# Optimization experiments

Hardware: AMD Instinct MI355X
Metric: run time of the kernel (lower is better)

Reference implementation:

```python
import jax, jax.numpy as jnp
import numpy as np

T, B, D, H = 1024, 256, 64, 128  # seq_len, batch, x_dim, dim_RNN (= dense dims)


def _linear_params(key, fan_in, fan_out):
    # torch nn.Linear/nn.RNN default init: U(-1/sqrt(fan_in), 1/sqrt(fan_in))
    s = 1.0 / np.sqrt(fan_in)
    kw, kb = jax.random.split(key)
    W = jax.random.uniform(kw, (fan_out, fan_in), minval=-s, maxval=s, dtype=jnp.float32)
    b = jax.random.uniform(kb, (fan_out,), minval=-s, maxval=s, dtype=jnp.float32)
    return W, b


def setup_inputs() -> dict:
    key = jax.random.key(0)
    kx, k1, k2, k3, k4, k5 = jax.random.split(key, 6)
    x = jax.random.normal(kx, (T, B, D), dtype=jnp.float32)
    W_x, b_x = _linear_params(k1, D, H)      # feature_extractor_x: Linear(D->H)
    W_ih, b_ih = _linear_params(k2, H, H)    # RNN input-hidden
    W_hh, b_hh = _linear_params(k3, H, H)    # RNN hidden-hidden
    W_h, b_h = _linear_params(k4, H, H)      # mlp_h_x: Linear(H->H)
    W_g, b_g = _linear_params(k5, H, D)      # gen_out: Linear(H->D)
    return {"x": x, "W_x": W_x, "b_x": b_x, "W_ih": W_ih, "b_ih": b_ih,
            "W_hh": W_hh, "b_hh": b_hh, "W_h": W_h, "b_h": b_h,
            "W_g": W_g, "b_g": b_g}


def reference(x, W_x, b_x, W_ih, b_ih, W_hh, b_hh, W_h, b_h, W_g, b_g):
    # feature extractor applied to all timesteps at once (as in the original)
    feat = jnp.tanh(x @ W_x.T + b_x)                       # [T, B, H]
    batch = x.shape[1]
    h0 = jnp.zeros((batch, W_hh.shape[0]), dtype=x.dtype)  # [B, H]

    def step(h, f_t):
        # y_t is produced from h BEFORE the recurrence update (y[0] uses h=0)
        y_t = jnp.tanh(h @ W_h.T + b_h) @ W_g.T + b_g      # [B, D]
        h_next = jnp.tanh(f_t @ W_ih.T + b_ih + h @ W_hh.T + b_hh)
        return h_next, y_t

    _, y = jax.lax.scan(step, h0, feat)                    # y: [T, B, D]
    return y
```

## Files before the change

### kernel.cpp

```cpp
#include <hip/hip_runtime.h>


#define T_SEQ 1024
#define B_SZ  256
#define D_IN  64
#define H_DIM 128

typedef __attribute__((ext_vector_type(8))) _Float16 half8;
typedef __attribute__((ext_vector_type(4))) _Float16 half4;
typedef __attribute__((ext_vector_type(4))) float f32x4;

__device__ __forceinline__ float fast_tanh(float x) {
  float ax = __builtin_fabsf(x);
  float e  = __builtin_amdgcn_exp2f(ax * -2.8853900817779268f);
  float r  = (1.0f - e) * __builtin_amdgcn_rcpf(1.0f + e);
  return __builtin_copysignf(r, x);
}

__device__ __forceinline__ void barrier_lds_only() {
  __asm__ __volatile__("" ::: "memory");
  __builtin_amdgcn_s_waitcnt(0xC07F);
  __builtin_amdgcn_s_barrier();
  __asm__ __volatile__("" ::: "memory");
}

__device__ __forceinline__ half8 pack_h8(float4 a, float4 b) {
  half8 s = { (_Float16)a.x, (_Float16)a.y, (_Float16)a.z, (_Float16)a.w,
              (_Float16)b.x, (_Float16)b.y, (_Float16)b.z, (_Float16)b.w };
  return s;
}

__device__ __forceinline__ float add_xor1(float x) {
  int v = __builtin_amdgcn_mov_dpp(__float_as_int(x), 0xB1, 0xF, 0xF, true);
  return x + __int_as_float(v);
}
__device__ __forceinline__ float add_xor2(float x) {
  int v = __builtin_amdgcn_mov_dpp(__float_as_int(x), 0x4E, 0xF, 0xF, true);
  return x + __int_as_float(v);
}
__device__ __forceinline__ float add_mirror8(float x) {
  int v = __builtin_amdgcn_mov_dpp(__float_as_int(x), 0x141, 0xF, 0xF, true);
  return x + __int_as_float(v);
}
__device__ __forceinline__ float dot4(float4 w, float4 h) {
  return fmaf(w.x, h.x, fmaf(w.y, h.y, fmaf(w.z, h.z, w.w * h.w)));
}

#define WI_S 136
#define XT_S 72
#define FM_S 136

__global__ __launch_bounds__(256) void k_feat_mfma(
    const float* __restrict__ x,  const float* __restrict__ Wx,
    const float* __restrict__ bx, const float* __restrict__ Wih,
    const float* __restrict__ bih,const float* __restrict__ bhh,
    float* __restrict__ Z)
{
  __shared__ __align__(16) _Float16 wi_l[128 * WI_S];
  __shared__ __align__(16) _Float16 xt_l[64 * XT_S];
  __shared__ __align__(16) _Float16 fm_l[64 * FM_S];

  const int tid = threadIdx.x;
  const int l   = tid & 63;
  const int wv  = tid >> 6;
  const int ln  = l & 15;
  const int kg  = l >> 4;

  {
    const float4* w4 = (const float4*)Wih;
#pragma unroll
    for (int p = 0; p < 16; ++p) {
      int f = tid + p * 256;
      int row = f >> 5, kc = (f & 31) * 4;
      float4 v = w4[f];
      half4 s = { (_Float16)v.x, (_Float16)v.y, (_Float16)v.z, (_Float16)v.w };
      *(half4*)&wi_l[row * WI_S + kc] = s;
    }
  }
  half8 wxr[8][2];
#pragma unroll
  for (int nt = 0; nt < 8; ++nt)
#pragma unroll
    for (int kf = 0; kf < 2; ++kf) {
      const float* wp = Wx + (nt*16 + ln) * D_IN + kf*32 + kg*8;
      wxr[nt][kf] = pack_h8(*(const float4*)wp, *(const float4*)(wp + 4));
    }

  float bx_r[8], b2_r[8];
#pragma unroll
  for (int nt = 0; nt < 8; ++nt) {
    bx_r[nt] = bx[nt*16 + ln];
    b2_r[nt] = bih[nt*16 + ln] + bhh[nt*16 + ln];
  }

  for (int it = 0; it < 8; ++it) {
    const long tile = blockIdx.x * 8 + it;
    const long r0   = tile * 64;

    {
      const float4* x4 = (const float4*)x;
#pragma unroll
      for (int p = 0; p < 4; ++p) {
        int f = tid + p * 256;
        int row = f >> 4, kc = (f & 15) * 4;
        float4 v = x4[r0 * 16 + f];
        half4 s = { (_Float16)v.x, (_Float16)v.y, (_Float16)v.z, (_Float16)v.w };
        *(half4*)&xt_l[row * XT_S + kc] = s;
      }
    }
    barrier_lds_only();

    half8 a1[2];
#pragma unroll
    for (int kf = 0; kf < 2; ++kf)
      a1[kf] = *(const half8*)&xt_l[(wv*16 + ln) * XT_S + kf*32 + kg*8];

#pragma unroll
    for (int nt = 0; nt < 8; ++nt) {
      f32x4 acc = {0.f, 0.f, 0.f, 0.f};
#pragma unroll
      for (int kf = 0; kf < 2; ++kf)
        acc = __builtin_amdgcn_mfma_f32_16x16x32_f16(a1[kf], wxr[nt][kf], acc, 0, 0, 0);
#pragma unroll
      for (int c = 0; c < 4; ++c) {
        float v = fast_tanh(acc[c] + bx_r[nt]);
        fm_l[(wv*16 + kg*4 + c) * FM_S + nt*16 + ln] = (_Float16)v;
      }
    }

    half8 a2[4];
#pragma unroll
    for (int kf = 0; kf < 4; ++kf)
      a2[kf] = *(const half8*)&fm_l[(wv*16 + ln) * FM_S + kf*32 + kg*8];

#pragma unroll
    for (int nt = 0; nt < 8; ++nt) {
      f32x4 acc = { b2_r[nt], b2_r[nt], b2_r[nt], b2_r[nt] };
#pragma unroll
      for (int kf = 0; kf < 4; ++kf) {
        half8 bf = *(const half8*)&wi_l[(nt*16 + ln) * WI_S + kf*32 + kg*8];
        acc = __builtin_amdgcn_mfma_f32_16x16x32_f16(a2[kf], bf, acc, 0, 0, 0);
      }
#pragma unroll
      for (int c = 0; c < 4; ++c)
        Z[(r0 + wv*16 + kg*4 + c) * H_DIM + nt*16 + ln] = acc[c];
    }
    barrier_lds_only();
  }
}

__global__ __launch_bounds__(256, 1) void k_scan(const float* __restrict__ Whh,
                                                 float* __restrict__ Z)
{
  __shared__ __align__(16) float hbuf[2][192];
  const int tid = threadIdx.x;
  const int b   = blockIdx.x;
  const int jg  = tid >> 3;
  const int ks  = tid & 7;
  const int k0p = ks * 24;

  float4 w[4][4];
#pragma unroll
  for (int r = 0; r < 4; ++r) {
    const float4* wg = (const float4*)(Whh + (jg + r*32)*H_DIM + ks*16);
#pragma unroll
    for (int m = 0; m < 4; ++m) w[r][m] = wg[m];
  }

  if (tid < 128) hbuf[0][tid + ((tid >> 4) << 3)] = 0.f;

  const bool writer = (ks < 4);
  const int  j_out  = jg + ks*32;
  const int  j_pad  = j_out + ((j_out >> 4) << 3);
  float* zp = Z + b*H_DIM + j_out;

  float zbuf[8];
#pragma unroll
  for (int i = 0; i < 8; ++i) zbuf[i] = writer ? zp[i * 32768] : 0.f;

  barrier_lds_only();

  for (int tb = 0; tb < T_SEQ; tb += 8) {
#pragma unroll
    for (int u = 0; u < 8; ++u) {
      const int t = tb + u;
      const float* h = hbuf[t & 1];
      float4 h0 = *(const float4*)&h[k0p];
      float4 h1 = *(const float4*)&h[k0p + 4];
      float4 h2 = *(const float4*)&h[k0p + 8];
      float4 h3 = *(const float4*)&h[k0p + 12];

      float a[4];
#pragma unroll
      for (int r = 0; r < 4; ++r) {
        float p0 = dot4(w[r][0], h0);
        float p1 = dot4(w[r][1], h1);
        float p2 = dot4(w[r][2], h2);
        float p3 = dot4(w[r][3], h3);
        a[r] = (p0 + p1) + (p2 + p3);
      }
#pragma unroll
      for (int r = 0; r < 4; ++r) {
        a[r] = add_xor1(a[r]);
        a[r] = add_xor2(a[r]);
        a[r] = add_mirror8(a[r]);
      }
      if (writer) {
        float v  = a[ks] + zbuf[u];
        float hn = fast_tanh(v);
        hbuf[(t & 1) ^ 1][j_pad] = hn;
        zp[t * 32768] = hn;
        zbuf[u] = (t + 8 < T_SEQ) ? zp[(t + 8) * 32768] : 0.f;
      }
      barrier_lds_only();
    }
  }
}

#define TILE_R 64
#define TPW    8
#define HM_S   136
#define WH_S   136

__global__ __launch_bounds__(256) void k_out_mfma(
    const float* __restrict__ Zh, const float* __restrict__ Wh,
    const float* __restrict__ bh, const float* __restrict__ Wg,
    const float* __restrict__ bg, float* __restrict__ y)
{
  __shared__ __align__(16) _Float16 wh_l[128 * WH_S];
  __shared__ __align__(16) _Float16 hm_l[TILE_R * HM_S];

  const int tid = threadIdx.x;
  const int l   = tid & 63;
  const int wv  = tid >> 6;
  const int ln  = l & 15;
  const int kg  = l >> 4;

  {
    const float4* wg4 = (const float4*)Wh;
#pragma unroll
    for (int p = 0; p < 16; ++p) {
      int f = tid + p * 256;
      int row = f >> 5, kc = (f & 31) * 4;
      float4 v = wg4[f];
      half4 s = { (_Float16)v.x, (_Float16)v.y, (_Float16)v.z, (_Float16)v.w };
      *(half4*)&wh_l[row * WH_S + kc] = s;
    }
  }

  half8 wg_r[4][4];
#pragma unroll
  for (int nt2 = 0; nt2 < 4; ++nt2)
#pragma unroll
    for (int ks = 0; ks < 4; ++ks) {
      const float* wp = Wg + (nt2*16 + ln) * H_DIM + ks*32 + kg*8;
      wg_r[nt2][ks] = pack_h8(*(const float4*)wp, *(const float4*)(wp + 4));
    }

  float bh_r[8], bg_r[4];
#pragma unroll
  for (int nt = 0; nt < 8; ++nt) bh_r[nt] = bh[nt*16 + ln];
#pragma unroll
  for (int nt2 = 0; nt2 < 4; ++nt2) bg_r[nt2] = bg[nt2*16 + ln];

  for (int it = 0; it < TPW; ++it) {
    const int tile = blockIdx.x * TPW + it;
    const long r0  = (long)tile * TILE_R;
    const bool zero = (tile < 4);

    {
      const float4* hg = (const float4*)(Zh + (r0 - 256) * H_DIM);
#pragma unroll
      for (int p = 0; p < 8; ++p) {
        int f = tid + p * 256;
        int row = f >> 5, kc = (f & 31) * 4;
        float4 v;
        if (zero) { v.x = v.y = v.z = v.w = 0.f; } else { v = hg[f]; }
        half4 s = { (_Float16)v.x, (_Float16)v.y, (_Float16)v.z, (_Float16)v.w };
        *(half4*)&hm_l[row * HM_S + kc] = s;
      }
    }
    barrier_lds_only();

    half8 af[4];
#pragma unroll
    for (int ks = 0; ks < 4; ++ks)
      af[ks] = *(const half8*)&hm_l[(wv*16 + ln) * HM_S + ks*32 + kg*8];

#pragma unroll
    for (int nt = 0; nt < 8; ++nt) {
      f32x4 acc = {0.f, 0.f, 0.f, 0.f};
#pragma unroll
      for (int ks = 0; ks < 4; ++ks) {
        half8 bf = *(const half8*)&wh_l[(nt*16 + ln) * WH_S + ks*32 + kg*8];
        acc = __builtin_amdgcn_mfma_f32_16x16x32_f16(af[ks], bf, acc, 0, 0, 0);
      }
#pragma unroll
      for (int c = 0; c < 4; ++c) {
        float val = fast_tanh(acc[c] + bh_r[nt]);
        hm_l[(wv*16 + kg*4 + c) * HM_S + nt*16 + ln] = (_Float16)val;
      }
    }

    half8 a2[4];
#pragma unroll
    for (int ks = 0; ks < 4; ++ks)
      a2[ks] = *(const half8*)&hm_l[(wv*16 + ln) * HM_S + ks*32 + kg*8];

#pragma unroll
    for (int nt2 = 0; nt2 < 4; ++nt2) {
      f32x4 acc2 = { bg_r[nt2], bg_r[nt2], bg_r[nt2], bg_r[nt2] };
#pragma unroll
      for (int ks = 0; ks < 4; ++ks)
        acc2 = __builtin_amdgcn_mfma_f32_16x16x32_f16(a2[ks], wg_r[nt2][ks],
                                                      acc2, 0, 0, 0);
#pragma unroll
      for (int c = 0; c < 4; ++c)
        y[(r0 + wv*16 + kg*4 + c) * D_IN + nt2*16 + ln] = acc2[c];
    }
    barrier_lds_only();
  }
}

extern "C" void kernel_launch(void* const* d_in, const int* in_sizes, int n_in,
                              void* d_out, int out_size, void* d_ws, size_t ws_size,
                              hipStream_t stream) {
  const float* x   = (const float*)d_in[0];
  const float* Wx  = (const float*)d_in[1];
  const float* bx  = (const float*)d_in[2];
  const float* Wih = (const float*)d_in[3];
  const float* bih = (const float*)d_in[4];
  const float* Whh = (const float*)d_in[5];
  const float* bhh = (const float*)d_in[6];
  const float* Wh  = (const float*)d_in[7];
  const float* bh  = (const float*)d_in[8];
  const float* Wg  = (const float*)d_in[9];
  const float* bg  = (const float*)d_in[10];
  float* Z = (float*)d_ws;
  float* y = (float*)d_out;

  k_feat_mfma<<<512, 256, 0, stream>>>(x, Wx, bx, Wih, bih, bhh, Z);
  k_scan     <<<B_SZ, 256, 0, stream>>>(Whh, Z);
  k_out_mfma <<<512, 256, 0, stream>>>(Z, Wh, bh, Wg, bg, y);
}
```

Baseline: 556.5 us.

## Split recurrent scan across 512 threads with one output row per quad

Reorganises the per-batch scan kernel so each block uses 512 threads. Each group of 4 lanes owns one hidden unit and splits the 128-long dot product into 4 chunks of 32. This replaces the old layout where 8 lanes each computed partial sums for 4 rows and reduced with three DPP steps. The reduction drops to two DPP adds and the per-thread dependent FMA chain gets shorter. In exchange each barrier now synchronises 8 waves instead of 4, there are more LDS reads per step, and only a quarter of the threads write results.

```diff
diff --git a/kernel.cpp b/kernel.cpp
--- a/kernel.cpp
+++ b/kernel.cpp
@@ -36,10 +36,6 @@
 }
 __device__ __forceinline__ float add_xor2(float x) {
   int v = __builtin_amdgcn_mov_dpp(__float_as_int(x), 0x4E, 0xF, 0xF, true);
-  return x + __int_as_float(v);
-}
-__device__ __forceinline__ float add_mirror8(float x) {
-  int v = __builtin_amdgcn_mov_dpp(__float_as_int(x), 0x141, 0xF, 0xF, true);
   return x + __int_as_float(v);
 }
 __device__ __forceinline__ float dot4(float4 w, float4 h) {
@@ -149,30 +145,27 @@
   }
 }
 
-__global__ __launch_bounds__(256, 1) void k_scan(const float* __restrict__ Whh,
+__global__ __launch_bounds__(512, 2) void k_scan(const float* __restrict__ Whh,
                                                  float* __restrict__ Z)
 {
-  __shared__ __align__(16) float hbuf[2][192];
+  __shared__ __align__(16) float hbuf[2][208];
   const int tid = threadIdx.x;
   const int b   = blockIdx.x;
-  const int jg  = tid >> 3;
-  const int ks  = tid & 7;
-  const int k0p = ks * 24;
-
-  float4 w[4][4];
-#pragma unroll
-  for (int r = 0; r < 4; ++r) {
-    const float4* wg = (const float4*)(Whh + (jg + r*32)*H_DIM + ks*16);
-#pragma unroll
-    for (int m = 0; m < 4; ++m) w[r][m] = wg[m];
-  }
-
-  if (tid < 128) hbuf[0][tid + ((tid >> 4) << 3)] = 0.f;
-
-  const bool writer = (ks < 4);
-  const int  j_out  = jg + ks*32;
-  const int  j_pad  = j_out + ((j_out >> 4) << 3);
-  float* zp = Z + b*H_DIM + j_out;
+  const int j   = tid >> 2;
+  const int ks  = tid & 3;
+  const int k0  = ks * 32;
+  const int k0p = ks * 56;
+
+  float4 w[8];
+#pragma unroll
+  for (int m = 0; m < 8; ++m)
+    w[m] = *(const float4*)(Whh + j*H_DIM + k0 + m*4);
+
+  if (tid < 128) hbuf[0][tid + ((tid >> 5) * 24)] = 0.f;
+
+  const bool writer = (ks == 0);
+  const int  jp     = j + ((j >> 5) * 24);
+  float* zp = Z + b*H_DIM + j;
 
   float zbuf[8];
 #pragma unroll
@@ -184,31 +177,33 @@
 #pragma unroll
     for (int u = 0; u < 8; ++u) {
       const int t = tb + u;
-      const float* h = hbuf[t & 1];
-      float4 h0 = *(const float4*)&h[k0p];
-      float4 h1 = *(const float4*)&h[k0p + 4];
-      float4 h2 = *(const float4*)&h[k0p + 8];
-      float4 h3 = *(const float4*)&h[k0p + 12];
-
-      float a[4];
-#pragma unroll
-      for (int r = 0; r < 4; ++r) {
-        float p0 = dot4(w[r][0], h0);
-        float p1 = dot4(w[r][1], h1);
-        float p2 = dot4(w[r][2], h2);
-        float p3 = dot4(w[r][3], h3);
-        a[r] = (p0 + p1) + (p2 + p3);
-      }
-#pragma unroll
-      for (int r = 0; r < 4; ++r) {
-        a[r] = add_xor1(a[r]);
-        a[r] = add_xor2(a[r]);
-        a[r] = add_mirror8(a[r]);
-      }
+      const float* h = hbuf[t & 1] + k0p;
+      float4 h0 = *(const float4*)(h);
+      float4 h1 = *(const float4*)(h + 4);
+      float4 h2 = *(const float4*)(h + 8);
+      float4 h3 = *(const float4*)(h + 12);
+      float4 h4 = *(const float4*)(h + 16);
+      float4 h5 = *(const float4*)(h + 20);
+      float4 h6 = *(const float4*)(h + 24);
+      float4 h7 = *(const float4*)(h + 28);
+
+      float p0 = dot4(w[0], h0);
+      float p1 = dot4(w[1], h1);
+      float p2 = dot4(w[2], h2);
+      float p3 = dot4(w[3], h3);
+      float p4 = dot4(w[4], h4);
+      float p5 = dot4(w[5], h5);
+      float p6 = dot4(w[6], h6);
+      float p7 = dot4(w[7], h7);
+      float a = ((p0 + p1) + (p2 + p3)) + ((p4 + p5) + (p6 + p7));
+
+      a = add_xor1(a);
+      a = add_xor2(a);
+
       if (writer) {
-        float v  = a[ks] + zbuf[u];
+        float v  = a + zbuf[u];
         float hn = fast_tanh(v);
-        hbuf[(t & 1) ^ 1][j_pad] = hn;
+        hbuf[(t & 1) ^ 1][jp] = hn;
         zp[t * 32768] = hn;
         zbuf[u] = (t + 8 < T_SEQ) ? zp[(t + 8) * 32768] : 0.f;
       }
@@ -340,6 +335,6 @@
   float* y = (float*)d_out;
 
   k_feat_mfma<<<512, 256, 0, stream>>>(x, Wx, bx, Wih, bih, bhh, Z);
-  k_scan     <<<B_SZ, 256, 0, stream>>>(Whh, Z);
+  k_scan     <<<B_SZ, 512, 0, stream>>>(Whh, Z);
   k_out_mfma <<<512, 256, 0, stream>>>(Z, Wh, bh, Wg, bg, y);
 }
```

Measured after the change: 546.3 us. No clear change (-1.8%).
